# Kernel optimization log

Measured on AMD Instinct MI355X. Metric: run time of the kernel, lower is better.

Reference implementation:

```python
import jax, jax.numpy as jnp
import numpy as np

K = 8192
D = 256


def setup_inputs() -> dict:
    key = jax.random.key(0)
    k1, k2 = jax.random.split(key)
    z_e_x = jax.random.normal(k1, (32, 32, 32, D), dtype=jnp.float32)
    # matches torch init: uniform(-1/K, 1/K)
    codebook = jax.random.uniform(k2, (K, D), dtype=jnp.float32,
                                  minval=-1.0 / K, maxval=1.0 / K)
    return {"z_e_x": z_e_x, "codebook": codebook}


def reference(z_e_x, codebook):
    # vq(): nearest-neighbor codebook indices under squared L2 distance.
    flat = z_e_x.reshape(-1, z_e_x.shape[-1])            # [N, D]
    # ||z - e||^2 = ||z||^2 - 2 z.e + ||e||^2 ; ||z||^2 constant over argmin
    dots = flat @ codebook.T                              # [N, K]
    cb_sq = jnp.sum(codebook * codebook, axis=-1)         # [K]
    dist = cb_sq[None, :] - 2.0 * dots                    # [N, K]
    indices = jnp.argmin(dist, axis=-1)                   # [N] int
    return indices.reshape(z_e_x.shape[:-1])              # latent index grid
```

## Files before the change

kernel.cpp:

```cpp
#include <hip/hip_runtime.h>
#include <hip/hip_fp16.h>


#define N_Q   32768
#define K_CB  8192
#define D_DIM 256

typedef _Float16 half8 __attribute__((ext_vector_type(8)));
typedef _Float16 half4 __attribute__((ext_vector_type(4)));
typedef float    f32x4 __attribute__((ext_vector_type(4)));

__device__ __forceinline__ void gl_lds16(const _Float16* g, _Float16* l) {
  __builtin_amdgcn_global_load_lds(
      (const __attribute__((address_space(1))) unsigned int*)g,
      (__attribute__((address_space(3))) unsigned int*)l, 16, 0, 0);
}

__global__ void vq_prep_z(const float* __restrict__ z,
                          _Float16* __restrict__ zh, _Float16* __restrict__ zl) {
  int i = blockIdx.x * 256 + threadIdx.x;
  float4 v = ((const float4*)z)[i];
  float xs[4] = {v.x * 16.0f, v.y * 16.0f, v.z * 16.0f, v.w * 16.0f};
  half4 h, l;
#pragma unroll
  for (int j = 0; j < 4; ++j) {
    _Float16 hj = (_Float16)xs[j];
    h[j] = hj;
    l[j] = (_Float16)(xs[j] - (float)hj);
  }
  ((half4*)zh)[i] = h;
  ((half4*)zl)[i] = l;
}

__global__ void vq_prep_cb(const float* __restrict__ cb,
                           _Float16* __restrict__ eh, _Float16* __restrict__ el,
                           float* __restrict__ cbs) {
  int w = threadIdx.x >> 6, lane = threadIdx.x & 63;
  int code = blockIdx.x * 4 + w;
  float4 v = ((const float4*)cb)[code * 64 + lane];
  float ss = v.x * v.x + v.y * v.y + v.z * v.z + v.w * v.w;
  float xs[4] = {v.x * 32768.0f, v.y * 32768.0f, v.z * 32768.0f, v.w * 32768.0f};
  half4 h, l;
#pragma unroll
  for (int j = 0; j < 4; ++j) {
    _Float16 hj = (_Float16)xs[j];
    h[j] = hj;
    l[j] = (_Float16)(xs[j] - (float)hj);
  }
  ((half4*)eh)[code * 64 + lane] = h;
  ((half4*)el)[code * 64 + lane] = l;
#pragma unroll
  for (int off = 1; off < 64; off <<= 1) ss += __shfl_xor(ss, off);
  if (lane == 0) cbs[code] = ss * 524288.0f;
}

__global__ __launch_bounds__(256, 2)
void vq_main(const _Float16* __restrict__ zh, const _Float16* __restrict__ zl,
             const _Float16* __restrict__ eh, const _Float16* __restrict__ el,
             const float* __restrict__ cbs,
             unsigned long long* __restrict__ partials) {
  __shared__ __align__(16) _Float16 Ah[8192], Al[8192], Bh[8192], Bl[8192];
  __shared__ float    redD[2][128];
  __shared__ unsigned redC[2][128];

  const int tid  = threadIdx.x;
  const int lane = tid & 63;
  const int w    = tid >> 6;
  const int q    = lane & 15;
  const int quad = lane >> 4;
  const int wrow = (w >> 1) * 64;
  const int wcol = (w & 1) * 64;

  const int qt    = blockIdx.x >> 1;
  const int split = blockIdx.x & 1;
  const int q0    = qt * 128;
  const int c0    = split * 4096;

  int offA[4][2], offB[4][2];
#pragma unroll
  for (int mt = 0; mt < 4; ++mt) {
    int ra = wrow + mt * 16 + q;
    int rb = wcol + mt * 16 + q;
#pragma unroll
    for (int k2 = 0; k2 < 2; ++k2) {
      int gb = k2 * 4 + quad;
      offA[mt][k2] = ra * 64 + ((gb ^ (ra & 7)) << 3);
      offB[mt][k2] = rb * 64 + ((gb ^ (rb & 7)) << 3);
    }
  }

  float    rd[16];
  unsigned rc[16];
#pragma unroll
  for (int i = 0; i < 16; ++i) { rd[i] = 3.0e38f; rc[i] = 0u; }

  for (int ct = 0; ct < 32; ++ct) {
    const int crow0 = c0 + ct * 128;
    f32x4 acc[4][4];
#pragma unroll
    for (int mt = 0; mt < 4; ++mt)
#pragma unroll
      for (int nt = 0; nt < 4; ++nt)
        acc[mt][nt] = (f32x4){0.f, 0.f, 0.f, 0.f};

    for (int kk = 0; kk < 4; ++kk) {
      const int kcol = kk * 64;
      __syncthreads();
#pragma unroll
      for (int c = 0; c < 4; ++c) {
        int bi   = (w * 4 + c) * 64 + lane;
        int row  = bi >> 3;
        int gb   = (bi & 7) ^ (row & 7);
        int goff = row * 256 + kcol + gb * 8;
        int ldst = (w * 4 + c) * 512;
        gl_lds16(zh + (size_t)q0 * 256 + goff,    &Ah[ldst]);
        gl_lds16(zl + (size_t)q0 * 256 + goff,    &Al[ldst]);
        gl_lds16(eh + (size_t)crow0 * 256 + goff, &Bh[ldst]);
        gl_lds16(el + (size_t)crow0 * 256 + goff, &Bl[ldst]);
      }
      __syncthreads();

#pragma unroll
      for (int k2 = 0; k2 < 2; ++k2) {
        half8 ahf[4], alf[4], bhf[4], blf[4];
#pragma unroll
        for (int i = 0; i < 4; ++i) {
          ahf[i] = *(const half8*)&Ah[offA[i][k2]];
          alf[i] = *(const half8*)&Al[offA[i][k2]];
          bhf[i] = *(const half8*)&Bh[offB[i][k2]];
          blf[i] = *(const half8*)&Bl[offB[i][k2]];
        }
#pragma unroll
        for (int mt = 0; mt < 4; ++mt)
#pragma unroll
          for (int nt = 0; nt < 4; ++nt) {
            acc[mt][nt] = __builtin_amdgcn_mfma_f32_16x16x32_f16(ahf[mt], bhf[nt], acc[mt][nt], 0, 0, 0);
            acc[mt][nt] = __builtin_amdgcn_mfma_f32_16x16x32_f16(ahf[mt], blf[nt], acc[mt][nt], 0, 0, 0);
            acc[mt][nt] = __builtin_amdgcn_mfma_f32_16x16x32_f16(alf[mt], bhf[nt], acc[mt][nt], 0, 0, 0);
          }
      }
    }

    const int cb0 = crow0 + wcol + q;
    float cbsv[4];
#pragma unroll
    for (int nt = 0; nt < 4; ++nt) cbsv[nt] = cbs[cb0 + nt * 16];
#pragma unroll
    for (int mt = 0; mt < 4; ++mt)
#pragma unroll
      for (int r = 0; r < 4; ++r) {
        float d = fmaf(-2.0f, acc[mt][0][r], cbsv[0]);
        unsigned cidx = (unsigned)cb0;
#pragma unroll
        for (int nt = 1; nt < 4; ++nt) {
          float dn = fmaf(-2.0f, acc[mt][nt][r], cbsv[nt]);
          if (dn < d) { d = dn; cidx = (unsigned)(cb0 + nt * 16); }
        }
        int ri = mt * 4 + r;
        if (d < rd[ri]) { rd[ri] = d; rc[ri] = cidx; }
      }
  }

#pragma unroll
  for (int ri = 0; ri < 16; ++ri) {
    float d = rd[ri]; unsigned cidx = rc[ri];
#pragma unroll
    for (int off = 1; off < 16; off <<= 1) {
      float od = __shfl_xor(d, off);
      unsigned oc = __shfl_xor(cidx, off);
      if (od < d || (od == d && oc < cidx)) { d = od; cidx = oc; }
    }
    if (q == 0) {
      int row = wrow + (ri >> 2) * 16 + quad * 4 + (ri & 3);
      redD[w & 1][row] = d;
      redC[w & 1][row] = cidx;
    }
  }
  __syncthreads();
  if (tid < 128) {
    float d0 = redD[0][tid]; unsigned cc0 = redC[0][tid];
    float d1 = redD[1][tid]; unsigned cc1 = redC[1][tid];
    if (d1 < d0 || (d1 == d0 && cc1 < cc0)) { d0 = d1; cc0 = cc1; }
    unsigned u = __float_as_uint(d0);
    u = (u & 0x80000000u) ? ~u : (u | 0x80000000u);
    partials[(size_t)split * N_Q + q0 + tid] = ((unsigned long long)u << 32) | cc0;
  }
}

__global__ void vq_final(const unsigned long long* __restrict__ partials,
                         int* __restrict__ out) {
  int i = blockIdx.x * 256 + threadIdx.x;
  unsigned long long a = partials[i], b = partials[(size_t)N_Q + i];
  unsigned long long m = (b < a) ? b : a;
  out[i] = (int)(unsigned)(m & 0xffffffffull);
}

extern "C" void kernel_launch(void* const* d_in, const int* in_sizes, int n_in,
                              void* d_out, int out_size, void* d_ws, size_t ws_size,
                              hipStream_t stream) {
  const float* z  = (const float*)d_in[0];
  const float* cb = (const float*)d_in[1];
  char* ws = (char*)d_ws;
  _Float16* zh = (_Float16*)(ws);
  _Float16* zl = (_Float16*)(ws + (size_t)16 * 1024 * 1024);
  _Float16* eh = (_Float16*)(ws + (size_t)32 * 1024 * 1024);
  _Float16* el = (_Float16*)(ws + (size_t)36 * 1024 * 1024);
  float*    cbs = (float*)(ws + (size_t)40 * 1024 * 1024);
  unsigned long long* partials =
      (unsigned long long*)(ws + (size_t)40 * 1024 * 1024 + 65536);

  hipLaunchKernelGGL(vq_prep_z,  dim3(8192), dim3(256), 0, stream, z, zh, zl);
  hipLaunchKernelGGL(vq_prep_cb, dim3(2048), dim3(256), 0, stream, cb, eh, el, cbs);
  hipLaunchKernelGGL(vq_main,    dim3(512),  dim3(256), 0, stream,
                     zh, zl, eh, el, cbs, partials);
  hipLaunchKernelGGL(vq_final,   dim3(128),  dim3(256), 0, stream,
                     partials, (int*)d_out);
}
```

Baseline: 444.3 us.

## Double-buffer LDS staging with 32-wide K chunks and prefetch next chunk

```diff
diff --git a/kernel.cpp b/kernel.cpp
--- a/kernel.cpp
+++ b/kernel.cpp
@@ -59,7 +59,8 @@
              const _Float16* __restrict__ eh, const _Float16* __restrict__ el,
              const float* __restrict__ cbs,
              unsigned long long* __restrict__ partials) {
-  __shared__ __align__(16) _Float16 Ah[8192], Al[8192], Bh[8192], Bl[8192];
+  __shared__ __align__(16) _Float16 Ah[2][4096], Al[2][4096];
+  __shared__ __align__(16) _Float16 Bh[2][4096], Bl[2][4096];
   __shared__ float    redD[2][128];
   __shared__ unsigned redC[2][128];
 
@@ -76,23 +77,46 @@
   const int q0    = qt * 128;
   const int c0    = split * 4096;
 
-  int offA[4][2], offB[4][2];
+  int srow[2], sgq[2], ldst[2];
+#pragma unroll
+  for (int c = 0; c < 2; ++c) {
+    int p   = (w * 2 + c) * 64 + lane;
+    srow[c] = p >> 2;
+    sgq[c]  = (p & 3) ^ ((srow[c] >> 1) & 3);
+    ldst[c] = (w * 2 + c) * 512;
+  }
+
+  const int sw = (quad ^ ((q >> 1) & 3)) << 3;
+  int offA[4], offB[4];
 #pragma unroll
   for (int mt = 0; mt < 4; ++mt) {
-    int ra = wrow + mt * 16 + q;
-    int rb = wcol + mt * 16 + q;
-#pragma unroll
-    for (int k2 = 0; k2 < 2; ++k2) {
-      int gb = k2 * 4 + quad;
-      offA[mt][k2] = ra * 64 + ((gb ^ (ra & 7)) << 3);
-      offB[mt][k2] = rb * 64 + ((gb ^ (rb & 7)) << 3);
-    }
+    offA[mt] = (wrow + mt * 16 + q) * 32 + sw;
+    offB[mt] = (wcol + mt * 16 + q) * 32 + sw;
   }
 
   float    rd[16];
   unsigned rc[16];
 #pragma unroll
   for (int i = 0; i < 16; ++i) { rd[i] = 3.0e38f; rc[i] = 0u; }
+
+  auto STAGE = [&](int sct, int skc, int pb) {
+    const int    kcol  = skc * 32;
+    const size_t abase = (size_t)q0 * 256 + kcol;
+    const size_t bbase = (size_t)(c0 + sct * 128) * 256 + kcol;
+#pragma unroll
+    for (int c = 0; c < 2; ++c) {
+      int goff = srow[c] * 256 + sgq[c] * 8;
+      gl_lds16(zh + abase + goff, &Ah[pb][ldst[c]]);
+      gl_lds16(zl + abase + goff, &Al[pb][ldst[c]]);
+      gl_lds16(eh + bbase + goff, &Bh[pb][ldst[c]]);
+      gl_lds16(el + bbase + goff, &Bl[pb][ldst[c]]);
+    }
+  };
+
+  STAGE(0, 0, 0);
+  asm volatile("s_waitcnt vmcnt(0)" ::: "memory");
+  __builtin_amdgcn_s_barrier();
+  __builtin_amdgcn_sched_barrier(0);
 
   for (int ct = 0; ct < 32; ++ct) {
     const int crow0 = c0 + ct * 128;
@@ -103,42 +127,37 @@
       for (int nt = 0; nt < 4; ++nt)
         acc[mt][nt] = (f32x4){0.f, 0.f, 0.f, 0.f};
 
-    for (int kk = 0; kk < 4; ++kk) {
-      const int kcol = kk * 64;
-      __syncthreads();
-#pragma unroll
-      for (int c = 0; c < 4; ++c) {
-        int bi   = (w * 4 + c) * 64 + lane;
-        int row  = bi >> 3;
-        int gb   = (bi & 7) ^ (row & 7);
-        int goff = row * 256 + kcol + gb * 8;
-        int ldst = (w * 4 + c) * 512;
-        gl_lds16(zh + (size_t)q0 * 256 + goff,    &Ah[ldst]);
-        gl_lds16(zl + (size_t)q0 * 256 + goff,    &Al[ldst]);
-        gl_lds16(eh + (size_t)crow0 * 256 + goff, &Bh[ldst]);
-        gl_lds16(el + (size_t)crow0 * 256 + goff, &Bl[ldst]);
+#pragma unroll
+    for (int kc = 0; kc < 8; ++kc) {
+      const int pb = kc & 1;
+      if (ct < 31 || kc < 7) {
+        const int ns = ct * 8 + kc + 1;
+        STAGE(ns >> 3, ns & 7, pb ^ 1);
       }
-      __syncthreads();
-
-#pragma unroll
-      for (int k2 = 0; k2 < 2; ++k2) {
-        half8 ahf[4], alf[4], bhf[4], blf[4];
-#pragma unroll
-        for (int i = 0; i < 4; ++i) {
-          ahf[i] = *(const half8*)&Ah[offA[i][k2]];
-          alf[i] = *(const half8*)&Al[offA[i][k2]];
-          bhf[i] = *(const half8*)&Bh[offB[i][k2]];
-          blf[i] = *(const half8*)&Bl[offB[i][k2]];
+
+      half8 ahf[4], alf[4], bhf[4], blf[4];
+#pragma unroll
+      for (int i = 0; i < 4; ++i) {
+        ahf[i] = *(const half8*)&Ah[pb][offA[i]];
+        alf[i] = *(const half8*)&Al[pb][offA[i]];
+        bhf[i] = *(const half8*)&Bh[pb][offB[i]];
+        blf[i] = *(const half8*)&Bl[pb][offB[i]];
+      }
+
+      __builtin_amdgcn_s_setprio(1);
+#pragma unroll
+      for (int mt = 0; mt < 4; ++mt)
+#pragma unroll
+        for (int nt = 0; nt < 4; ++nt) {
+          acc[mt][nt] = __builtin_amdgcn_mfma_f32_16x16x32_f16(ahf[mt], bhf[nt], acc[mt][nt], 0, 0, 0);
+          acc[mt][nt] = __builtin_amdgcn_mfma_f32_16x16x32_f16(ahf[mt], blf[nt], acc[mt][nt], 0, 0, 0);
+          acc[mt][nt] = __builtin_amdgcn_mfma_f32_16x16x32_f16(alf[mt], bhf[nt], acc[mt][nt], 0, 0, 0);
         }
-#pragma unroll
-        for (int mt = 0; mt < 4; ++mt)
-#pragma unroll
-          for (int nt = 0; nt < 4; ++nt) {
-            acc[mt][nt] = __builtin_amdgcn_mfma_f32_16x16x32_f16(ahf[mt], bhf[nt], acc[mt][nt], 0, 0, 0);
-            acc[mt][nt] = __builtin_amdgcn_mfma_f32_16x16x32_f16(ahf[mt], blf[nt], acc[mt][nt], 0, 0, 0);
-            acc[mt][nt] = __builtin_amdgcn_mfma_f32_16x16x32_f16(alf[mt], bhf[nt], acc[mt][nt], 0, 0, 0);
-          }
-      }
+      __builtin_amdgcn_s_setprio(0);
+
+      asm volatile("s_waitcnt vmcnt(0)" ::: "memory");
+      __builtin_amdgcn_s_barrier();
+      __builtin_amdgcn_sched_barrier(0);
     }
 
     const int cb0 = crow0 + wcol + q;
```

New measurement: 599.3 us. 34.9% more time.
